# Kernel optimization log

Measured on AMD Instinct MI355X. Metric: run time of the kernel, lower is better.

Reference implementation:

```python
import jax, jax.numpy as jnp
import numpy as np

EPS = 1e-12  # torch F.normalize eps

def setup_inputs() -> dict:
    key = jax.random.key(0)
    k1, k2, k3 = jax.random.split(key, 3)
    b, c, h, w = 4, 192, 128, 128
    x = jax.random.normal(k1, (b, c, h, w), dtype=jnp.float32)
    # torch Linear weight transposed: x @ W_qkv, columns ordered [q | k | v]
    W_qkv = jax.random.normal(k2, (c, 3 * c), dtype=jnp.float32) * (1.0 / np.sqrt(c))
    W_lin = jax.random.normal(k3, (c, c), dtype=jnp.float32) * (1.0 / np.sqrt(c))
    sigma = jnp.ones((1, 1), dtype=jnp.float32)
    return {"x": x, "W_qkv": W_qkv, "W_lin": W_lin, "sigma": sigma}

def _l2norm_tokens(t):
    # normalize along token axis (dim=1 of [b, hw, c]), torch-style eps clamp
    n = jnp.sqrt(jnp.sum(t * t, axis=1, keepdims=True))
    return t / jnp.maximum(n, EPS)

def reference(x, W_qkv, W_lin, sigma):
    b, c, h, w = x.shape
    xt = jnp.transpose(x.reshape(b, c, h * w), (0, 2, 1))  # [b, hw, c]
    qkv = xt @ W_qkv                                        # [b, hw, 3c]
    q, k, v = jnp.split(qkv, 3, axis=-1)
    q = _l2norm_tokens(q)
    k = _l2norm_tokens(k)
    attn = jnp.einsum('bnc,bnd->bcd', k, q) * sigma[0, 0]   # [b, c, c]
    attn = jax.nn.softmax(attn, axis=-1)
    out = jnp.einsum('bnc,bcd->bnd', v, attn) @ W_lin       # [b, hw, c]
    return jnp.transpose(out, (0, 2, 1)).reshape(b, c, h, w)
```

## Files before the change

### kernel.cpp

```cpp
#include <hip/hip_runtime.h>

#define CCH 192
#define HWN 16384
#define NB  4
#define SPLIT 16

typedef __attribute__((ext_vector_type(8))) short bf16x8;
typedef __attribute__((ext_vector_type(4))) float f32x4;


__device__ __forceinline__ ushort f2bf(float f) {
  union { float f; unsigned u; } v; v.f = f;
  return (ushort)((v.u + 0x7fffu + ((v.u >> 16) & 1u)) >> 16);
}

__device__ __forceinline__ float wsum(float v) {
#pragma unroll
  for (int off = 32; off > 0; off >>= 1) v += __shfl_xor(v, off, 64);
  return v;
}
__device__ __forceinline__ float wmax(float v) {
#pragma unroll
  for (int off = 32; off > 0; off >>= 1) v = fmaxf(v, __shfl_xor(v, off, 64));
  return v;
}

__global__ __launch_bounds__(256) void k0_wconv(const float* __restrict__ Wqkv, ushort* __restrict__ Wb) {
  int j0 = blockIdx.x * 64, c0 = blockIdx.y * 64;
  __shared__ float L[64][65];
  int t = threadIdx.x;
#pragma unroll
  for (int p = 0; p < 4; ++p) {
    int idx = t + 256 * p;
    int row = idx >> 4, col = (idx & 15) << 2;
    float4 v = *reinterpret_cast<const float4*>(&Wqkv[(size_t)(c0 + row) * 576 + j0 + col]);
    L[row][col] = v.x; L[row][col + 1] = v.y; L[row][col + 2] = v.z; L[row][col + 3] = v.w;
  }
  __syncthreads();
#pragma unroll
  for (int p = 0; p < 4; ++p) {
    int idx = t + 256 * p;
    int jrow = idx >> 4, c4 = (idx & 15) << 2;
    ushort4 o;
    o.x = f2bf(L[c4 + 0][jrow]);
    o.y = f2bf(L[c4 + 1][jrow]);
    o.z = f2bf(L[c4 + 2][jrow]);
    o.w = f2bf(L[c4 + 3][jrow]);
    *reinterpret_cast<ushort4*>(&Wb[(size_t)(j0 + jrow) * CCH + c0 + c4]) = o;
  }
}

__global__ __launch_bounds__(256) void k1_xpose(const float* __restrict__ x, ushort* __restrict__ xT2) {
  int z = blockIdx.z;
  const float* xb = x + (size_t)z * CCH * HWN;
  ushort* xb2 = xT2 + (size_t)z * HWN * CCH;
  int n0 = blockIdx.x * 64, c0 = blockIdx.y * 64;
  __shared__ float L[64][65];
  int t = threadIdx.x;
#pragma unroll
  for (int p = 0; p < 4; ++p) {
    int idx = t + 256 * p;
    int row = idx >> 4, col = (idx & 15) << 2;
    float4 v = *reinterpret_cast<const float4*>(&xb[(size_t)(c0 + row) * HWN + n0 + col]);
    L[row][col] = v.x; L[row][col + 1] = v.y; L[row][col + 2] = v.z; L[row][col + 3] = v.w;
  }
  __syncthreads();
#pragma unroll
  for (int p = 0; p < 2; ++p) {
    int idx = t + 256 * p;
    int nq = idx & 15, cg = (idx >> 4) & 7, n16 = idx >> 7;
    int nl = n16 * 16 + nq;
    unsigned u0 = (unsigned)f2bf(L[cg * 8 + 0][nl]) | ((unsigned)f2bf(L[cg * 8 + 1][nl]) << 16);
    unsigned u1 = (unsigned)f2bf(L[cg * 8 + 2][nl]) | ((unsigned)f2bf(L[cg * 8 + 3][nl]) << 16);
    unsigned u2 = (unsigned)f2bf(L[cg * 8 + 4][nl]) | ((unsigned)f2bf(L[cg * 8 + 5][nl]) << 16);
    unsigned u3 = (unsigned)f2bf(L[cg * 8 + 6][nl]) | ((unsigned)f2bf(L[cg * 8 + 7][nl]) << 16);
    size_t off = (size_t)((n0 >> 4) + n16) * (16 * CCH) + ((c0 >> 3) + cg) * 128 + nq * 8;
    *reinterpret_cast<int4*>(&xb2[off]) = make_int4(u0, u1, u2, u3);
  }
}

__global__ __launch_bounds__(256) void k2_qkv(
    const ushort* __restrict__ xT2, const ushort* __restrict__ Wb,
    ushort* __restrict__ Tqk2, ushort* __restrict__ Vt2, float* __restrict__ norm2p)
{
  int z = blockIdx.z;
  const ushort* xb2 = xT2 + (size_t)z * HWN * CCH;
  ushort* Tb2 = Tqk2 + (size_t)z * 384 * HWN;
  ushort* Vb2 = Vt2 + (size_t)z * HWN * CCH;
  float* npb = norm2p + (size_t)z * 256 * 384;
  int nt = blockIdx.x, jt = blockIdx.y;
  int n0 = nt * 128, j0 = jt * 64;
  __shared__ __align__(16) ushort Ep[9216];
  int t = threadIdx.x, l = t & 63, w = t >> 6;
  int wn = w >> 1, wj = w & 1, lg = l >> 4, lr = l & 15;
  int nblk = n0 >> 4;
  bf16x8 bfrag[2][3][2];
#pragma unroll
  for (int h = 0; h < 2; ++h)
#pragma unroll
    for (int k3 = 0; k3 < 3; ++k3)
#pragma unroll
      for (int f = 0; f < 2; ++f)
        bfrag[h][k3][f] = *reinterpret_cast<const bf16x8*>(
            &Wb[(size_t)(j0 + 32 * wj + 16 * f + lr) * CCH + 96 * h + 32 * k3 + 8 * lg]);
  f32x4 acc[4][2] = {};
#pragma unroll
  for (int h = 0; h < 2; ++h)
#pragma unroll
    for (int k3 = 0; k3 < 3; ++k3) {
      bf16x8 a[4];
#pragma unroll
      for (int m = 0; m < 4; ++m)
        a[m] = *reinterpret_cast<const bf16x8*>(
            &xb2[(size_t)(nblk + 4 * wn + m) * (16 * CCH) + (12 * h + 4 * k3 + lg) * 128 + lr * 8]);
#pragma unroll
      for (int m = 0; m < 4; ++m)
#pragma unroll
        for (int f = 0; f < 2; ++f)
          acc[m][f] = __builtin_amdgcn_mfma_f32_16x16x32_bf16(a[m], bfrag[h][k3][f], acc[m][f], 0, 0, 0);
    }
  if (jt >= 6) {
#pragma unroll
    for (int m = 0; m < 4; ++m)
#pragma unroll
      for (int f = 0; f < 2; ++f) {
        int cl = 32 * wj + 16 * f + lr;
#pragma unroll
        for (int r = 0; r < 4; ++r)
          Ep[(64 * wn + 16 * m + 4 * lg + r) * 72 + cl] = f2bf(acc[m][f][r]);
      }
    __syncthreads();
    int cb8 = (jt - 6) * 8;
#pragma unroll
    for (int p = 0; p < 4; ++p) {
      int idx = t + 256 * p;
      int nq = idx & 15, cg = (idx >> 4) & 7, n16 = idx >> 7;
      int4 v = *reinterpret_cast<const int4*>(&Ep[(n16 * 16 + nq) * 72 + cg * 8]);
      size_t off = (size_t)(nblk + n16) * (16 * CCH) + (cb8 + cg) * 128 + nq * 8;
      *reinterpret_cast<int4*>(&Vb2[off]) = v;
    }
  } else {
    int jb = j0 + 32 * wj;
#pragma unroll
    for (int f = 0; f < 2; ++f) {
      float sq = 0.f;
      int j = jb + 16 * f + lr;
#pragma unroll
      for (int m = 0; m < 4; ++m)
#pragma unroll
        for (int r = 0; r < 4; ++r) sq += acc[m][f][r] * acc[m][f][r];
      sq += __shfl_xor(sq, 16, 64);
      sq += __shfl_xor(sq, 32, 64);
      if (lg == 0) npb[(size_t)(2 * nt + wn) * 384 + j] = sq;
    }
#pragma unroll
    for (int m = 0; m < 4; ++m)
#pragma unroll
      for (int f = 0; f < 2; ++f) {
        int jl = 32 * wj + 16 * f + lr;
        int nb = 64 * wn + 16 * m + 4 * lg;
        unsigned p0 = (unsigned)f2bf(acc[m][f][0]) | ((unsigned)f2bf(acc[m][f][1]) << 16);
        unsigned p1 = (unsigned)f2bf(acc[m][f][2]) | ((unsigned)f2bf(acc[m][f][3]) << 16);
        *reinterpret_cast<unsigned*>(&Ep[jl * 136 + nb]) = p0;
        *reinterpret_cast<unsigned*>(&Ep[jl * 136 + nb + 2]) = p1;
      }
    __syncthreads();
#pragma unroll
    for (int p = 0; p < 4; ++p) {
      int idx = t + 256 * p;
      int jq = idx & 15, nc = (idx >> 4) & 15, jb16 = idx >> 8;
      int4 v = *reinterpret_cast<const int4*>(&Ep[(jb16 * 16 + jq) * 136 + nc * 8]);
      size_t off = (size_t)((j0 >> 4) + jb16) * (16 * HWN) + ((n0 >> 3) + nc) * 128 + jq * 8;
      *reinterpret_cast<int4*>(&Tb2[off]) = v;
    }
  }
}

__global__ __launch_bounds__(256) void k3_invn(const float* __restrict__ norm2p, float* __restrict__ invn) {
  int z = blockIdx.y, j = blockIdx.x;
  const float* npb = norm2p + (size_t)z * 256 * 384;
  int t = threadIdx.x;
  float s = npb[(size_t)t * 384 + j];
  s = wsum(s);
  __shared__ float red[4];
  if ((t & 63) == 0) red[t >> 6] = s;
  __syncthreads();
  if (t == 0) {
    float tot = red[0] + red[1] + red[2] + red[3];
    invn[(size_t)z * 384 + j] = 1.f / fmaxf(sqrtf(tot), 1e-12f);
  }
}

__global__ __launch_bounds__(256) void k4_gram(const ushort* __restrict__ Tqk2, float* __restrict__ Gpart) {
  int z = blockIdx.z;
  const ushort* Tb2 = Tqk2 + (size_t)z * 384 * HWN;
  float* Gb = Gpart + (size_t)z * SPLIT * CCH * CCH;
  int tile = blockIdx.x, chunk = blockIdx.y;
  int ct = tile / 3, dt = tile % 3;
  int t = threadIdx.x, l = t & 63, w = t >> 6;
  int wc = w >> 1, wd = w & 1, lg = l >> 4, lr = l & 15;
  f32x4 acc[2][2] = {};
  for (int s = 0; s < 16; ++s) {
    int nco = chunk * 128 + s * 8;
#pragma unroll
    for (int hh = 0; hh < 2; ++hh) {
      int ko = nco + 4 * hh + lg;
      bf16x8 a[2], bb[2];
#pragma unroll
      for (int m = 0; m < 2; ++m)
        a[m] = *reinterpret_cast<const bf16x8*>(
            &Tb2[(size_t)(12 + 4 * ct + 2 * wc + m) * (16 * HWN) + ko * 128 + lr * 8]);
#pragma unroll
      for (int f = 0; f < 2; ++f)
        bb[f] = *reinterpret_cast<const bf16x8*>(
            &Tb2[(size_t)(4 * dt + 2 * wd + f) * (16 * HWN) + ko * 128 + lr * 8]);
#pragma unroll
      for (int m = 0; m < 2; ++m)
#pragma unroll
        for (int f = 0; f < 2; ++f)
          acc[m][f] = __builtin_amdgcn_mfma_f32_16x16x32_bf16(a[m], bb[f], acc[m][f], 0, 0, 0);
    }
  }
#pragma unroll
  for (int m = 0; m < 2; ++m)
#pragma unroll
    for (int f = 0; f < 2; ++f)
#pragma unroll
      for (int r = 0; r < 4; ++r)
        Gb[(size_t)(chunk * CCH + ct * 64 + 32 * wc + 16 * m + 4 * lg + r) * CCH +
           dt * 64 + 32 * wd + 16 * f + lr] = acc[m][f][r];
}

__global__ __launch_bounds__(64) void k5_softmax(
    const float* __restrict__ Gpart, const float* __restrict__ invn,
    const float* __restrict__ sigma, float* __restrict__ S)
{
  int c = blockIdx.x, z = blockIdx.y;
  const float* Gb = Gpart + (size_t)z * SPLIT * CCH * CCH;
  const float* inb = invn + (size_t)z * 384;
  float sig = sigma[0];
  float ink = inb[192 + c];
  float lv[3];
#pragma unroll
  for (int r = 0; r < 3; ++r) {
    int d = threadIdx.x + 64 * r;
    float s = 0.f;
    for (int ch = 0; ch < SPLIT; ++ch)
      s += Gb[(size_t)(ch * CCH + c) * CCH + d];
    lv[r] = s * ink * inb[d] * sig;
  }
  float m = fmaxf(lv[0], fmaxf(lv[1], lv[2]));
  m = wmax(m);
  float e[3], tot = 0.f;
#pragma unroll
  for (int r = 0; r < 3; ++r) { e[r] = __expf(lv[r] - m); tot += e[r]; }
  tot = wsum(tot);
  float inv = 1.f / tot;
  float* Sb = S + (size_t)z * CCH * CCH;
#pragma unroll
  for (int r = 0; r < 3; ++r) Sb[(size_t)c * CCH + threadIdx.x + 64 * r] = e[r] * inv;
}

__global__ __launch_bounds__(192) void k6_mlin(
    const float* __restrict__ S, const float* __restrict__ Wlin, ushort* __restrict__ Mt)
{
  int z = blockIdx.y, c = blockIdx.x, e = threadIdx.x;
  const float* Sb = S + (size_t)z * CCH * CCH;
  float s = 0.f;
  for (int d = 0; d < CCH; ++d) s += Sb[(size_t)c * CCH + d] * Wlin[(size_t)d * CCH + e];
  Mt[(size_t)z * CCH * CCH + (size_t)e * CCH + c] = f2bf(s);
}

__global__ __launch_bounds__(256) void k7_out(
    const ushort* __restrict__ Mt, const ushort* __restrict__ Vt2, float* __restrict__ out)
{
  int z = blockIdx.z;
  const ushort* Mb = Mt + (size_t)z * CCH * CCH;
  const ushort* Vb2 = Vt2 + (size_t)z * HWN * CCH;
  float* ob = out + (size_t)z * CCH * HWN;
  int nt = blockIdx.x, et = blockIdx.y;
  int e0 = et * 64, n0 = nt * 128;
  int t = threadIdx.x, l = t & 63, w = t >> 6;
  int wn = w >> 1, we = w & 1, lg = l >> 4, lr = l & 15;
  int nblk = n0 >> 4;
  bf16x8 mfrag[2][3][2];
#pragma unroll
  for (int h = 0; h < 2; ++h)
#pragma unroll
    for (int k3 = 0; k3 < 3; ++k3)
#pragma unroll
      for (int mg = 0; mg < 2; ++mg)
        mfrag[h][k3][mg] = *reinterpret_cast<const bf16x8*>(
            &Mb[(size_t)(e0 + 32 * we + 16 * mg + lr) * CCH + 96 * h + 32 * k3 + 8 * lg]);
  f32x4 acc[4][2] = {};
#pragma unroll
  for (int h = 0; h < 2; ++h)
#pragma unroll
    for (int k3 = 0; k3 < 3; ++k3) {
      bf16x8 an[4];
#pragma unroll
      for (int ng = 0; ng < 4; ++ng)
        an[ng] = *reinterpret_cast<const bf16x8*>(
            &Vb2[(size_t)(nblk + 4 * wn + ng) * (16 * CCH) + (12 * h + 4 * k3 + lg) * 128 + lr * 8]);
#pragma unroll
      for (int ng = 0; ng < 4; ++ng)
#pragma unroll
        for (int mg = 0; mg < 2; ++mg)
          acc[ng][mg] = __builtin_amdgcn_mfma_f32_16x16x32_bf16(an[ng], mfrag[h][k3][mg], acc[ng][mg], 0, 0, 0);
    }
#pragma unroll
  for (int ng = 0; ng < 4; ++ng)
#pragma unroll
    for (int mg = 0; mg < 2; ++mg)
      *reinterpret_cast<f32x4*>(
          &ob[(size_t)(e0 + 32 * we + 16 * mg + lr) * HWN + n0 + 64 * wn + 16 * ng + 4 * lg]) = acc[ng][mg];
}

extern "C" void kernel_launch(void* const* d_in, const int* in_sizes, int n_in,
                              void* d_out, int out_size, void* d_ws, size_t ws_size,
                              hipStream_t stream) {
  const float* x     = (const float*)d_in[0];
  const float* Wqkv  = (const float*)d_in[1];
  const float* Wlin  = (const float*)d_in[2];
  const float* sigma = (const float*)d_in[3];
  float* out = (float*)d_out;

  const size_t wbElems = (size_t)576 * CCH;
  const size_t perB =
      (size_t)HWN * CCH * 2 +
      (size_t)384 * HWN * 2 +
      (size_t)HWN * CCH * 2 +
      (size_t)256 * 384 * 4 +
      (size_t)384 * 4 +
      (size_t)SPLIT * CCH * CCH * 4 +
      (size_t)CCH * CCH * 4 +
      (size_t)CCH * CCH * 2;
  int per = (ws_size >= wbElems * 2 + (size_t)NB * perB) ? NB : 1;

  ushort* Wb = (ushort*)d_ws;
  k0_wconv<<<dim3(9, 3), 256, 0, stream>>>(Wqkv, Wb);

  for (int b0 = 0; b0 < NB; b0 += per) {
    char* base = (char*)d_ws + wbElems * 2;
    ushort* xT2  = (ushort*)base;
    ushort* Tqk2 = xT2 + (size_t)per * HWN * CCH;
    ushort* Vt2  = Tqk2 + (size_t)per * 384 * HWN;
    float* norm2p = (float*)(Vt2 + (size_t)per * HWN * CCH);
    float* invn  = norm2p + (size_t)per * 256 * 384;
    float* Gpart = invn + (size_t)per * 384;
    float* S     = Gpart + (size_t)per * SPLIT * CCH * CCH;
    ushort* Mt   = (ushort*)(S + (size_t)per * CCH * CCH);
    const float* xb = x + (size_t)b0 * CCH * HWN;
    float* ob = out + (size_t)b0 * CCH * HWN;

    k1_xpose  <<<dim3(256, 3, per), 256, 0, stream>>>(xb, xT2);
    k2_qkv    <<<dim3(128, 9, per), 256, 0, stream>>>(xT2, Wb, Tqk2, Vt2, norm2p);
    k3_invn   <<<dim3(384, per), 256, 0, stream>>>(norm2p, invn);
    k4_gram   <<<dim3(9, SPLIT, per), 256, 0, stream>>>(Tqk2, Gpart);
    k5_softmax<<<dim3(192, per), 64, 0, stream>>>(Gpart, invn, sigma, S);
    k6_mlin   <<<dim3(192, per), 192, 0, stream>>>(S, Wlin, Mt);
    k7_out    <<<dim3(128, 3, per), 256, 0, stream>>>(Mt, Vt2, ob);
  }
}
```

Baseline: 131.6 us.

## Fuse x transpose/bf16 conversion into QKV projection kernel via shared memory

```diff
diff --git a/kernel.cpp b/kernel.cpp
--- a/kernel.cpp
+++ b/kernel.cpp
@@ -50,114 +50,110 @@
   }
 }
 
-__global__ __launch_bounds__(256) void k1_xpose(const float* __restrict__ x, ushort* __restrict__ xT2) {
-  int z = blockIdx.z;
-  const float* xb = x + (size_t)z * CCH * HWN;
-  ushort* xb2 = xT2 + (size_t)z * HWN * CCH;
-  int n0 = blockIdx.x * 64, c0 = blockIdx.y * 64;
-  __shared__ float L[64][65];
-  int t = threadIdx.x;
-#pragma unroll
-  for (int p = 0; p < 4; ++p) {
-    int idx = t + 256 * p;
-    int row = idx >> 4, col = (idx & 15) << 2;
-    float4 v = *reinterpret_cast<const float4*>(&xb[(size_t)(c0 + row) * HWN + n0 + col]);
-    L[row][col] = v.x; L[row][col + 1] = v.y; L[row][col + 2] = v.z; L[row][col + 3] = v.w;
-  }
-  __syncthreads();
-#pragma unroll
-  for (int p = 0; p < 2; ++p) {
-    int idx = t + 256 * p;
-    int nq = idx & 15, cg = (idx >> 4) & 7, n16 = idx >> 7;
-    int nl = n16 * 16 + nq;
-    unsigned u0 = (unsigned)f2bf(L[cg * 8 + 0][nl]) | ((unsigned)f2bf(L[cg * 8 + 1][nl]) << 16);
-    unsigned u1 = (unsigned)f2bf(L[cg * 8 + 2][nl]) | ((unsigned)f2bf(L[cg * 8 + 3][nl]) << 16);
-    unsigned u2 = (unsigned)f2bf(L[cg * 8 + 4][nl]) | ((unsigned)f2bf(L[cg * 8 + 5][nl]) << 16);
-    unsigned u3 = (unsigned)f2bf(L[cg * 8 + 6][nl]) | ((unsigned)f2bf(L[cg * 8 + 7][nl]) << 16);
-    size_t off = (size_t)((n0 >> 4) + n16) * (16 * CCH) + ((c0 >> 3) + cg) * 128 + nq * 8;
-    *reinterpret_cast<int4*>(&xb2[off]) = make_int4(u0, u1, u2, u3);
-  }
-}
-
-__global__ __launch_bounds__(256) void k2_qkv(
-    const ushort* __restrict__ xT2, const ushort* __restrict__ Wb,
+__global__ __launch_bounds__(512, 4) void k12_qkv(
+    const float* __restrict__ x, const ushort* __restrict__ Wb,
     ushort* __restrict__ Tqk2, ushort* __restrict__ Vt2, float* __restrict__ norm2p)
 {
   int z = blockIdx.z;
-  const ushort* xb2 = xT2 + (size_t)z * HWN * CCH;
+  const float* xb = x + (size_t)z * CCH * HWN;
   ushort* Tb2 = Tqk2 + (size_t)z * 384 * HWN;
   ushort* Vb2 = Vt2 + (size_t)z * HWN * CCH;
   float* npb = norm2p + (size_t)z * 256 * 384;
-  int nt = blockIdx.x, jt = blockIdx.y;
-  int n0 = nt * 128, j0 = jt * 64;
-  __shared__ __align__(16) ushort Ep[9216];
+  int jt = blockIdx.x;
+  int nt = blockIdx.y;
+  int n0 = nt * 128;
+  __shared__ __align__(16) ushort SM[28800];
+  ushort* FR = SM;
+  ushort* LT = SM + 24576;
   int t = threadIdx.x, l = t & 63, w = t >> 6;
-  int wn = w >> 1, wj = w & 1, lg = l >> 4, lr = l & 15;
-  int nblk = n0 >> 4;
-  bf16x8 bfrag[2][3][2];
-#pragma unroll
-  for (int h = 0; h < 2; ++h)
-#pragma unroll
-    for (int k3 = 0; k3 < 3; ++k3)
-#pragma unroll
-      for (int f = 0; f < 2; ++f)
-        bfrag[h][k3][f] = *reinterpret_cast<const bf16x8*>(
-            &Wb[(size_t)(j0 + 32 * wj + 16 * f + lr) * CCH + 96 * h + 32 * k3 + 8 * lg]);
-  f32x4 acc[4][2] = {};
-#pragma unroll
-  for (int h = 0; h < 2; ++h)
-#pragma unroll
-    for (int k3 = 0; k3 < 3; ++k3) {
-      bf16x8 a[4];
-#pragma unroll
-      for (int m = 0; m < 4; ++m)
-        a[m] = *reinterpret_cast<const bf16x8*>(
-            &xb2[(size_t)(nblk + 4 * wn + m) * (16 * CCH) + (12 * h + 4 * k3 + lg) * 128 + lr * 8]);
-#pragma unroll
-      for (int m = 0; m < 4; ++m)
-#pragma unroll
-        for (int f = 0; f < 2; ++f)
-          acc[m][f] = __builtin_amdgcn_mfma_f32_16x16x32_bf16(a[m], bfrag[h][k3][f], acc[m][f], 0, 0, 0);
-    }
-  if (jt >= 6) {
+  int wn = w >> 2, wj = w & 3, lg = l >> 4, lr = l & 15;
+
+  for (int tile = 0; tile < 6; ++tile) {
+    int c0 = tile * 32;
+#pragma unroll
+    for (int p = 0; p < 2; ++p) {
+      int ii = t + 512 * p;
+      int c = ii >> 5, nf4 = ii & 31;
+      float4 v = *reinterpret_cast<const float4*>(&xb[(size_t)(c0 + c) * HWN + n0 + 4 * nf4]);
+      ushort4 o; o.x = f2bf(v.x); o.y = f2bf(v.y); o.z = f2bf(v.z); o.w = f2bf(v.w);
+      *reinterpret_cast<ushort4*>(&LT[c * 132 + 4 * nf4]) = o;
+    }
+    __syncthreads();
+    {
+      int cchunk = t >> 7, nl = t & 127;
+      unsigned q0 = LT[(cchunk * 8 + 0) * 132 + nl] | ((unsigned)LT[(cchunk * 8 + 1) * 132 + nl] << 16);
+      unsigned q1 = LT[(cchunk * 8 + 2) * 132 + nl] | ((unsigned)LT[(cchunk * 8 + 3) * 132 + nl] << 16);
+      unsigned q2 = LT[(cchunk * 8 + 4) * 132 + nl] | ((unsigned)LT[(cchunk * 8 + 5) * 132 + nl] << 16);
+      unsigned q3 = LT[(cchunk * 8 + 6) * 132 + nl] | ((unsigned)LT[(cchunk * 8 + 7) * 132 + nl] << 16);
+      int chunk = (c0 >> 3) + cchunk;
+      *reinterpret_cast<int4*>(&FR[(nl >> 4) * 3072 + chunk * 128 + (nl & 15) * 8]) =
+          make_int4(q0, q1, q2, q3);
+    }
+    __syncthreads();
+  }
+
+  f32x4 acc[4][3] = {};
+#pragma unroll
+  for (int k = 0; k < 6; ++k) {
+    bf16x8 a[4], b[3];
 #pragma unroll
     for (int m = 0; m < 4; ++m)
-#pragma unroll
-      for (int f = 0; f < 2; ++f) {
-        int cl = 32 * wj + 16 * f + lr;
+      a[m] = *reinterpret_cast<const bf16x8*>(&FR[(4 * wn + m) * 3072 + (4 * k + lg) * 128 + lr * 8]);
+#pragma unroll
+    for (int f = 0; f < 3; ++f)
+      b[f] = *reinterpret_cast<const bf16x8*>(
+          &Wb[(size_t)(jt * 192 + wj * 48 + 16 * f + lr) * CCH + 32 * k + 8 * lg]);
+#pragma unroll
+    for (int m = 0; m < 4; ++m)
+#pragma unroll
+      for (int f = 0; f < 3; ++f)
+        acc[m][f] = __builtin_amdgcn_mfma_f32_16x16x32_bf16(a[m], b[f], acc[m][f], 0, 0, 0);
+  }
+  __syncthreads();
+
+  if (jt == 2) {
+    ushort* Ep = SM;
+#pragma unroll
+    for (int m = 0; m < 4; ++m)
+#pragma unroll
+      for (int f = 0; f < 3; ++f) {
+        int cl = wj * 48 + 16 * f + lr;
+        int nb = 64 * wn + 16 * m + 4 * lg;
 #pragma unroll
         for (int r = 0; r < 4; ++r)
-          Ep[(64 * wn + 16 * m + 4 * lg + r) * 72 + cl] = f2bf(acc[m][f][r]);
+          Ep[(nb + r) * 200 + cl] = f2bf(acc[m][f][r]);
       }
     __syncthreads();
-    int cb8 = (jt - 6) * 8;
-#pragma unroll
-    for (int p = 0; p < 4; ++p) {
-      int idx = t + 256 * p;
-      int nq = idx & 15, cg = (idx >> 4) & 7, n16 = idx >> 7;
-      int4 v = *reinterpret_cast<const int4*>(&Ep[(n16 * 16 + nq) * 72 + cg * 8]);
-      size_t off = (size_t)(nblk + n16) * (16 * CCH) + (cb8 + cg) * 128 + nq * 8;
+    int nblk = n0 >> 4;
+#pragma unroll
+    for (int p = 0; p < 6; ++p) {
+      int ii = t + 512 * p;
+      int nq = ii & 15, n16 = ii / 384, cg = (ii - n16 * 384) >> 4;
+      int4 v = *reinterpret_cast<const int4*>(&Ep[(n16 * 16 + nq) * 200 + cg * 8]);
+      size_t off = (size_t)(nblk + n16) * (16 * CCH) + cg * 128 + nq * 8;
       *reinterpret_cast<int4*>(&Vb2[off]) = v;
     }
   } else {
-    int jb = j0 + 32 * wj;
-#pragma unroll
-    for (int f = 0; f < 2; ++f) {
+#pragma unroll
+    for (int f = 0; f < 3; ++f) {
       float sq = 0.f;
-      int j = jb + 16 * f + lr;
 #pragma unroll
       for (int m = 0; m < 4; ++m)
 #pragma unroll
         for (int r = 0; r < 4; ++r) sq += acc[m][f][r] * acc[m][f][r];
       sq += __shfl_xor(sq, 16, 64);
       sq += __shfl_xor(sq, 32, 64);
-      if (lg == 0) npb[(size_t)(2 * nt + wn) * 384 + j] = sq;
-    }
+      if (lg == 0) {
+        int j = jt * 192 + wj * 48 + 16 * f + lr;
+        npb[(size_t)(2 * nt + wn) * 384 + j] = sq;
+      }
+    }
+    ushort* Ep = SM;
 #pragma unroll
     for (int m = 0; m < 4; ++m)
 #pragma unroll
-      for (int f = 0; f < 2; ++f) {
-        int jl = 32 * wj + 16 * f + lr;
+      for (int f = 0; f < 3; ++f) {
+        int jl = wj * 48 + 16 * f + lr;
         int nb = 64 * wn + 16 * m + 4 * lg;
         unsigned p0 = (unsigned)f2bf(acc[m][f][0]) | ((unsigned)f2bf(acc[m][f][1]) << 16);
         unsigned p1 = (unsigned)f2bf(acc[m][f][2]) | ((unsigned)f2bf(acc[m][f][3]) << 16);
@@ -166,11 +162,11 @@
       }
     __syncthreads();
 #pragma unroll
-    for (int p = 0; p < 4; ++p) {
-      int idx = t + 256 * p;
-      int jq = idx & 15, nc = (idx >> 4) & 15, jb16 = idx >> 8;
+    for (int p = 0; p < 6; ++p) {
+      int ii = t + 512 * p;
+      int jq = ii & 15, nc = (ii >> 4) & 15, jb16 = ii >> 8;
       int4 v = *reinterpret_cast<const int4*>(&Ep[(jb16 * 16 + jq) * 136 + nc * 8]);
-      size_t off = (size_t)((j0 >> 4) + jb16) * (16 * HWN) + ((n0 >> 3) + nc) * 128 + jq * 8;
+      size_t off = (size_t)(jt * 12 + jb16) * (16 * HWN) + ((size_t)(n0 >> 3) + nc) * 128 + jq * 8;
       *reinterpret_cast<int4*>(&Tb2[off]) = v;
     }
   }
@@ -209,11 +205,11 @@
 #pragma unroll
       for (int m = 0; m < 2; ++m)
         a[m] = *reinterpret_cast<const bf16x8*>(
-            &Tb2[(size_t)(12 + 4 * ct + 2 * wc + m) * (16 * HWN) + ko * 128 + lr * 8]);
+            &Tb2[(size_t)(12 + 4 * ct + 2 * wc + m) * (16 * HWN) + (size_t)ko * 128 + lr * 8]);
 #pragma unroll
       for (int f = 0; f < 2; ++f)
         bb[f] = *reinterpret_cast<const bf16x8*>(
-            &Tb2[(size_t)(4 * dt + 2 * wd + f) * (16 * HWN) + ko * 128 + lr * 8]);
+            &Tb2[(size_t)(4 * dt + 2 * wd + f) * (16 * HWN) + (size_t)ko * 128 + lr * 8]);
 #pragma unroll
       for (int m = 0; m < 2; ++m)
 #pragma unroll
@@ -271,7 +267,7 @@
   Mt[(size_t)z * CCH * CCH + (size_t)e * CCH + c] = f2bf(s);
 }
 
-__global__ __launch_bounds__(256) void k7_out(
+__global__ __launch_bounds__(256, 2) void k7_out(
     const ushort* __restrict__ Mt, const ushort* __restrict__ Vt2, float* __restrict__ out)
 {
   int z = blockIdx.z;
@@ -327,7 +323,6 @@
 
   const size_t wbElems = (size_t)576 * CCH;
   const size_t perB =
-      (size_t)HWN * CCH * 2 +
       (size_t)384 * HWN * 2 +
       (size_t)HWN * CCH * 2 +
       (size_t)256 * 384 * 4 +
@@ -342,8 +337,7 @@
 
   for (int b0 = 0; b0 < NB; b0 += per) {
     char* base = (char*)d_ws + wbElems * 2;
-    ushort* xT2  = (ushort*)base;
-    ushort* Tqk2 = xT2 + (size_t)per * HWN * CCH;
+    ushort* Tqk2 = (ushort*)base;
     ushort* Vt2  = Tqk2 + (size_t)per * 384 * HWN;
     float* norm2p = (float*)(Vt2 + (size_t)per * HWN * CCH);
     float* invn  = norm2p + (size_t)per * 256 * 384;
@@ -353,8 +347,7 @@
     const float* xb = x + (size_t)b0 * CCH * HWN;
     float* ob = out + (size_t)b0 * CCH * HWN;
 
-    k1_xpose  <<<dim3(256, 3, per), 256, 0, stream>>>(xb, xT2);
-    k2_qkv    <<<dim3(128, 9, per), 256, 0, stream>>>(xT2, Wb, Tqk2, Vt2, norm2p);
+    k12_qkv   <<<dim3(3, 128, per), 512, 0, stream>>>(xb, Wb, Tqk2, Vt2, norm2p);
     k3_invn   <<<dim3(384, per), 256, 0, stream>>>(norm2p, invn);
     k4_gram   <<<dim3(9, SPLIT, per), 256, 0, stream>>>(Tqk2, Gpart);
     k5_softmax<<<dim3(192, per), 64, 0, stream>>>(Gpart, invn, sigma, S);
```

Result: no change. 130.0 us (-1.2%).
